# Optimization experiments

Measured on AMD Instinct MI355X. Metric: run time of the kernel, lower is better.

Reference implementation:

```python
import jax, jax.numpy as jnp
import numpy as np

P = 16         # patch size
D = 192        # embed dim (vit_tiny)
NH = 3         # heads
DEPTH = 12
HID = 768      # mlp hidden = 4*D
NCLS = 1000
PCT = 0.25
EPS = 1e-6


def _ln(x, s, b):
    m = x.mean(-1, keepdims=True)
    v = ((x - m) ** 2).mean(-1, keepdims=True)
    return (x - m) * jax.lax.rsqrt(v + EPS) * s + b


def setup_inputs() -> dict:
    key = jax.random.key(0)
    ks = jax.random.split(key, 24)
    B, IMG = 64, 384
    std = 0.02
    d = {
        "magno_image": jax.random.normal(ks[0], (B, 3, IMG, IMG), jnp.float32),
        "line_drawing": jax.random.uniform(ks[1], (B, 1, IMG, IMG), jnp.float32),
        "conv_w": jax.random.normal(ks[2], (D, 3, P, P), jnp.float32) * std,
        "conv_b": jnp.zeros((D,), jnp.float32),
        "pos_embed": jax.random.normal(ks[3], (1, (IMG // P) ** 2 + 1, D), jnp.float32) * std,
        "cls_token": jax.random.normal(ks[4], (1, 1, D), jnp.float32) * std,
        "ln1_s": jnp.ones((DEPTH, D), jnp.float32),
        "ln1_b": jnp.zeros((DEPTH, D), jnp.float32),
        "qkv_w": jax.random.normal(ks[5], (DEPTH, D, 3 * D), jnp.float32) * std,
        "qkv_b": jnp.zeros((DEPTH, 3 * D), jnp.float32),
        "proj_w": jax.random.normal(ks[6], (DEPTH, D, D), jnp.float32) * std,
        "proj_b": jnp.zeros((DEPTH, D), jnp.float32),
        "ln2_s": jnp.ones((DEPTH, D), jnp.float32),
        "ln2_b": jnp.zeros((DEPTH, D), jnp.float32),
        "fc1_w": jax.random.normal(ks[7], (DEPTH, D, HID), jnp.float32) * std,
        "fc1_b": jnp.zeros((DEPTH, HID), jnp.float32),
        "fc2_w": jax.random.normal(ks[8], (DEPTH, HID, D), jnp.float32) * std,
        "fc2_b": jnp.zeros((DEPTH, D), jnp.float32),
        "normf_s": jnp.ones((D,), jnp.float32),
        "normf_b": jnp.zeros((D,), jnp.float32),
        "head_w": jax.random.normal(ks[9], (D, NCLS), jnp.float32) * std,
        "head_b": jnp.zeros((NCLS,), jnp.float32),
    }
    return d


def _forward(magno_image, line_drawing, conv_w, conv_b, pos_embed, cls_token,
             ln1_s, ln1_b, qkv_w, qkv_b, proj_w, proj_b, ln2_s, ln2_b,
             fc1_w, fc1_b, fc2_w, fc2_b, normf_s, normf_b, head_w, head_b):
    B, _, IMG, _ = magno_image.shape
    g = IMG // P
    N = g * g
    k = int(N * PCT)
    hd = D // NH

    # --- PatchImportanceScorer: avg-pool(patch_size) then flatten ---
    scores = line_drawing.reshape(B, g, P, g, P).mean(axis=(2, 4)).reshape(B, N)

    # --- patch embed (conv stride == kernel == reshaped matmul) ---
    x = magno_image.reshape(B, 3, g, P, g, P).transpose(0, 2, 4, 1, 3, 5)
    patches = x.reshape(B, N, 3 * P * P) @ conv_w.reshape(D, 3 * P * P).T + conv_b

    # --- top_k selection + gather of patches and pos-embed ---
    _, idx = jax.lax.top_k(scores, k)                      # (B, k)
    sel = jnp.take_along_axis(patches, idx[:, :, None], axis=1)
    pos = jnp.take_along_axis(
        jnp.broadcast_to(pos_embed[:, 1:, :], (B, N, D)), idx[:, :, None], axis=1)
    sel = sel + pos

    cls = jnp.broadcast_to(cls_token + pos_embed[:, :1, :], (B, 1, D))
    seq = jnp.concatenate([cls, sel], axis=1)              # (B, 1+k, D)
    S = 1 + k

    def block(h, p):
        l1s, l1b, qw, qb, pw, pb, l2s, l2b, f1w, f1b, f2w, f2b = p
        y = _ln(h, l1s, l1b)
        qkv = (y @ qw + qb).reshape(B, S, 3, NH, hd)
        q, kk, v = qkv[:, :, 0], qkv[:, :, 1], qkv[:, :, 2]  # (B,S,NH,hd)
        att = jnp.einsum('bqhd,bkhd->bhqk', q, kk) / np.sqrt(hd).astype(np.float32)
        att = jax.nn.softmax(att, axis=-1)
        o = jnp.einsum('bhqk,bkhd->bqhd', att, v).reshape(B, S, D)
        h = h + o @ pw + pb
        y = _ln(h, l2s, l2b)
        h = h + jax.nn.gelu(y @ f1w + f1b, approximate=False) @ f2w + f2b
        return h, None

    seq, _ = jax.lax.scan(block, seq, (ln1_s, ln1_b, qkv_w, qkv_b, proj_w, proj_b,
                                       ln2_s, ln2_b, fc1_w, fc1_b, fc2_w, fc2_b))
    seq = _ln(seq, normf_s, normf_b)
    return seq[:, 0] @ head_w + head_b


def reference(magno_image, line_drawing, conv_w, conv_b, pos_embed, cls_token,
              ln1_s, ln1_b, qkv_w, qkv_b, proj_w, proj_b, ln2_s, ln2_b,
              fc1_w, fc1_b, fc2_w, fc2_b, normf_s, normf_b, head_w, head_b):
    return _forward(magno_image, line_drawing, conv_w, conv_b, pos_embed, cls_token,
                    ln1_s, ln1_b, qkv_w, qkv_b, proj_w, proj_b, ln2_s, ln2_b,
                    fc1_w, fc1_b, fc2_w, fc2_b, normf_s, normf_b, head_w, head_b)
```

## Files before the change

### kernel.cpp

```cpp
#include <hip/hip_runtime.h>
#include <hip/hip_bf16.h>
#include <cmath>


#define Bsz   64
#define NPATCH 576
#define KSEL  144
#define SEQ   145
#define DIM   192
#define HIDN  768

typedef __bf16 bf16x8 __attribute__((ext_vector_type(8)));
typedef float  f32x4  __attribute__((ext_vector_type(4)));

__global__ __launch_bounds__(256) void scores_kernel(const float* __restrict__ line,
                                                     float* __restrict__ scores)
{
    int gp = blockIdx.x;
    int b = gp / NPATCH, p = gp % NPATCH;
    int gy = p / 24, gx = p % 24;
    int t = threadIdx.x, py = t >> 4, px = t & 15;
    float v = line[((size_t)b * 384 + gy * 16 + py) * 384 + gx * 16 + px];
    for (int off = 32; off; off >>= 1) v += __shfl_xor(v, off);
    __shared__ float red[4];
    if ((t & 63) == 0) red[t >> 6] = v;
    __syncthreads();
    if (t == 0) scores[gp] = (red[0] + red[1] + red[2] + red[3]) * (1.f / 256.f);
}

__global__ __launch_bounds__(256) void topk_kernel(const float* __restrict__ scores,
                                                   int* __restrict__ idx)
{
    int b = blockIdx.x;
    __shared__ float s[NPATCH];
    for (int i = threadIdx.x; i < NPATCH; i += 256) s[i] = scores[b * NPATCH + i];
    __syncthreads();
    for (int i = threadIdx.x; i < NPATCH; i += 256) {
        float si = s[i];
        int cnt = 0;
        for (int j = 0; j < NPATCH; ++j) {
            float sj = s[j];
            cnt += (sj > si) || (sj == si && j < i);
        }
        if (cnt < KSEL) idx[b * KSEL + cnt] = i;
    }
}

__global__ __launch_bounds__(256) void gather_kernel(const float* __restrict__ magno,
                                                     const int* __restrict__ idx,
                                                     __hip_bfloat16* __restrict__ selp)
{
    int bs = blockIdx.x;
    int b = bs / KSEL;
    int pi = idx[bs];
    int gy = pi / 24, gx = pi % 24;
    int t = threadIdx.x, py = t >> 4, px = t & 15;
    size_t src = ((size_t)b * 3 * 384 + gy * 16 + py) * 384 + gx * 16 + px;
    __hip_bfloat16* dst = &selp[(size_t)bs * 768];
#pragma unroll
    for (int c = 0; c < 3; ++c)
        dst[c * 256 + t] = __float2bfloat16(magno[src + (size_t)c * 384 * 384]);
}

__global__ __launch_bounds__(256) void convert_bf16_kernel(const float* __restrict__ src,
                                                           __hip_bfloat16* __restrict__ dst,
                                                           int n)
{
    int i = blockIdx.x * 256 + threadIdx.x;
    if (i < n) dst[i] = __float2bfloat16(src[i]);
}

__global__ __launch_bounds__(256) void transpose_w_kernel(const float* __restrict__ src,
                                                          __hip_bfloat16* __restrict__ dst,
                                                          int R, int C)
{
    __shared__ float t[32][33];
    size_t lo = (size_t)blockIdx.z * R * C;
    int r0 = blockIdx.y * 32, c0 = blockIdx.x * 32;
    int tx = threadIdx.x & 31, ty = threadIdx.x >> 5;
#pragma unroll
    for (int i = 0; i < 32; i += 8)
        t[ty + i][tx] = src[lo + (size_t)(r0 + ty + i) * C + c0 + tx];
    __syncthreads();
#pragma unroll
    for (int i = 0; i < 32; i += 8)
        dst[lo + (size_t)(c0 + ty + i) * R + r0 + tx] = __float2bfloat16(t[tx][ty + i]);
}

__global__ void cls_kernel(const float* __restrict__ cls, const float* __restrict__ pos,
                           float* __restrict__ h)
{
    int b = blockIdx.x, t = threadIdx.x;
    h[(size_t)b * SEQ * DIM + t] = cls[t] + pos[t];
}

__global__ __launch_bounds__(256) void ln_kernel(const float* __restrict__ x,
                                                 const float* __restrict__ s,
                                                 const float* __restrict__ bia,
                                                 __hip_bfloat16* __restrict__ y, int ntok)
{
    int w = threadIdx.x >> 6, lane = threadIdx.x & 63;
    int tok = blockIdx.x * 4 + w;
    if (tok >= ntok) return;
    const float* xp = &x[(size_t)tok * DIM];
    float x0 = xp[lane], x1 = xp[lane + 64], x2 = xp[lane + 128];
    float sum = x0 + x1 + x2;
    for (int off = 32; off; off >>= 1) sum += __shfl_xor(sum, off);
    float mean = sum * (1.f / 192.f);
    float d0 = x0 - mean, d1 = x1 - mean, d2 = x2 - mean;
    float vs = d0 * d0 + d1 * d1 + d2 * d2;
    for (int off = 32; off; off >>= 1) vs += __shfl_xor(vs, off);
    float rs = rsqrtf(vs * (1.f / 192.f) + 1e-6f);
    __hip_bfloat16* yp = &y[(size_t)tok * DIM];
    yp[lane]       = __float2bfloat16(d0 * rs * s[lane]       + bia[lane]);
    yp[lane + 64]  = __float2bfloat16(d1 * rs * s[lane + 64]  + bia[lane + 64]);
    yp[lane + 128] = __float2bfloat16(d2 * rs * s[lane + 128] + bia[lane + 128]);
}

__global__ __launch_bounds__(256) void gemm_embed(const __hip_bfloat16* __restrict__ A,
                                                  const __hip_bfloat16* __restrict__ Wt,
                                                  const float* __restrict__ bias,
                                                  float* __restrict__ h,
                                                  int K,
                                                  const int* __restrict__ selidx,
                                                  const float* __restrict__ pos)
{
    __shared__ __align__(16) char As[8192];
    __shared__ __align__(16) char Bs[8192];
    const int tid = threadIdx.x;
    const int lane = tid & 63, wid = tid >> 6;
    const int wr = wid >> 1, wc = wid & 1;
    const int lr = lane & 15, lk = lane >> 4;
    const int m0 = blockIdx.y * 64, n0 = blockIdx.x * 64;
    f32x4 acc[2][2] = {};

    for (int k0 = 0; k0 < K; k0 += 64) {
#pragma unroll
        for (int it = 0; it < 2; ++it) {
            int chunk = it * 256 + tid;
            int r = chunk >> 3, g = chunk & 7;
            int loff = r * 128 + ((g ^ (r & 7)) * 16);
            *reinterpret_cast<uint4*>(As + loff) =
                *reinterpret_cast<const uint4*>(&A[(size_t)(m0 + r) * K + k0 + g * 8]);
            *reinterpret_cast<uint4*>(Bs + loff) =
                *reinterpret_cast<const uint4*>(&Wt[(size_t)(n0 + r) * K + k0 + g * 8]);
        }
        __syncthreads();
#pragma unroll
        for (int kc = 0; kc < 2; ++kc) {
            int g = kc * 4 + lk;
            bf16x8 af[2], bfr[2];
#pragma unroll
            for (int mi = 0; mi < 2; ++mi) {
                int r = wr * 32 + mi * 16 + lr;
                af[mi] = *reinterpret_cast<const bf16x8*>(As + r * 128 + ((g ^ (r & 7)) * 16));
            }
#pragma unroll
            for (int ni = 0; ni < 2; ++ni) {
                int r = wc * 32 + ni * 16 + lr;
                bfr[ni] = *reinterpret_cast<const bf16x8*>(Bs + r * 128 + ((g ^ (r & 7)) * 16));
            }
#pragma unroll
            for (int mi = 0; mi < 2; ++mi)
#pragma unroll
                for (int ni = 0; ni < 2; ++ni)
                    acc[mi][ni] = __builtin_amdgcn_mfma_f32_16x16x32_bf16(
                        af[mi], bfr[ni], acc[mi][ni], 0, 0, 0);
        }
        __syncthreads();
    }

#pragma unroll
    for (int mi = 0; mi < 2; ++mi)
#pragma unroll
    for (int ni = 0; ni < 2; ++ni)
#pragma unroll
    for (int j = 0; j < 4; ++j) {
        int row = m0 + wr * 32 + mi * 16 + (lane >> 4) * 4 + j;
        int col = n0 + wc * 32 + ni * 16 + (lane & 15);
        float v = acc[mi][ni][j] + bias[col];
        int bb2 = row / KSEL, ss = row % KSEL;
        int pi = selidx[row];
        v += pos[(size_t)(1 + pi) * DIM + col];
        h[((size_t)bb2 * SEQ + 1 + ss) * DIM + col] = v;
    }
}

__global__ __launch_bounds__(256) void gemm_qkv(const __hip_bfloat16* __restrict__ A,
                                                const __hip_bfloat16* __restrict__ Wt,
                                                const float* __restrict__ bias,
                                                __hip_bfloat16* __restrict__ qk,
                                                __hip_bfloat16* __restrict__ Vt)
{
    __shared__ __align__(16) char As[8192];
    __shared__ __align__(16) char Bs[8192];
    const int tid = threadIdx.x;
    const int lane = tid & 63, wid = tid >> 6;
    const int wr = wid >> 1, wc = wid & 1;
    const int lr = lane & 15, lk = lane >> 4;
    const int m0 = blockIdx.y * 64, n0 = blockIdx.x * 64;
    const int K = DIM;
    f32x4 acc[2][2] = {};

    for (int k0 = 0; k0 < K; k0 += 64) {
#pragma unroll
        for (int it = 0; it < 2; ++it) {
            int chunk = it * 256 + tid;
            int r = chunk >> 3, g = chunk & 7;
            int loff = r * 128 + ((g ^ (r & 7)) * 16);
            *reinterpret_cast<uint4*>(As + loff) =
                *reinterpret_cast<const uint4*>(&A[(size_t)(m0 + r) * K + k0 + g * 8]);
            *reinterpret_cast<uint4*>(Bs + loff) =
                *reinterpret_cast<const uint4*>(&Wt[(size_t)(n0 + r) * K + k0 + g * 8]);
        }
        __syncthreads();
#pragma unroll
        for (int kc = 0; kc < 2; ++kc) {
            int g = kc * 4 + lk;
            bf16x8 af[2], bfr[2];
#pragma unroll
            for (int mi = 0; mi < 2; ++mi) {
                int r = wr * 32 + mi * 16 + lr;
                af[mi] = *reinterpret_cast<const bf16x8*>(As + r * 128 + ((g ^ (r & 7)) * 16));
            }
#pragma unroll
            for (int ni = 0; ni < 2; ++ni) {
                int r = wc * 32 + ni * 16 + lr;
                bfr[ni] = *reinterpret_cast<const bf16x8*>(Bs + r * 128 + ((g ^ (r & 7)) * 16));
            }
#pragma unroll
            for (int mi = 0; mi < 2; ++mi)
#pragma unroll
                for (int ni = 0; ni < 2; ++ni)
                    acc[mi][ni] = __builtin_amdgcn_mfma_f32_16x16x32_bf16(
                        af[mi], bfr[ni], acc[mi][ni], 0, 0, 0);
        }
        __syncthreads();
    }

#pragma unroll
    for (int mi = 0; mi < 2; ++mi)
#pragma unroll
    for (int ni = 0; ni < 2; ++ni)
#pragma unroll
    for (int j = 0; j < 4; ++j) {
        int row = m0 + wr * 32 + mi * 16 + (lane >> 4) * 4 + j;
        int col = n0 + wc * 32 + ni * 16 + (lane & 15);
        float v = acc[mi][ni][j] + bias[col];
        if (col < 384) {
            qk[(size_t)row * 384 + col] = __float2bfloat16(v);
        } else {
            int c = col - 384;
            int b = row / SEQ, s = row - b * SEQ;
            Vt[((size_t)(b * 3 + (c >> 6)) * 64 + (c & 63)) * 160 + s] = __float2bfloat16(v);
        }
    }
}

__global__ __launch_bounds__(512) void attnproj_fc1_kernel(
    const __hip_bfloat16* __restrict__ qk,
    const __hip_bfloat16* __restrict__ Vt,
    const __hip_bfloat16* __restrict__ Wp,
    const float* __restrict__ pbias,
    float* __restrict__ h,
    const float* __restrict__ ls,
    const float* __restrict__ lb,
    const __hip_bfloat16* __restrict__ W1t,
    const float* __restrict__ b1,
    __hip_bfloat16* __restrict__ tbuf)
{
    const int b = blockIdx.y, qt = blockIdx.x;
    const int tid = threadIdx.x;
    const int w = tid >> 6, lane = tid & 63;
    const int lr = lane & 15, lg = lane >> 4;
    __shared__ __hip_bfloat16 Ps[3][32][168];
    __shared__ __hip_bfloat16 Ot[32][200];
    __shared__ float redsum[4][32];
    __shared__ float redsq[4][32];
    __hip_bfloat16* Yt = &Ps[0][0][0];

    const size_t qbase = (size_t)b * SEQ * 384;
    const int q0 = qt * 32;

    if (w < 6) {
        const int hh = w >> 1, half = w & 1;
        const int qrow = q0 + half * 16;
        bf16x8 aq[2];
#pragma unroll
        for (int ks = 0; ks < 2; ++ks)
            aq[ks] = *reinterpret_cast<const bf16x8*>(
                &qk[qbase + (size_t)(qrow + lr) * 384 + hh * 64 + ks * 32 + lg * 8]);
        f32x4 sc[10] = {};
#pragma unroll
        for (int nf = 0; nf < 10; ++nf) {
            int key = nf * 16 + lr;
#pragma unroll
            for (int ks = 0; ks < 2; ++ks) {
                bf16x8 bk = *reinterpret_cast<const bf16x8*>(
                    &qk[qbase + (size_t)key * 384 + 192 + hh * 64 + ks * 32 + lg * 8]);
                sc[nf] = __builtin_amdgcn_mfma_f32_16x16x32_bf16(aq[ks], bk, sc[nf], 0, 0, 0);
            }
        }
        float mx[4] = {-1e30f, -1e30f, -1e30f, -1e30f};
#pragma unroll
        for (int nf = 0; nf < 10; ++nf) {
            bool valid = nf * 16 + lr < SEQ;
#pragma unroll
            for (int j = 0; j < 4; ++j) {
                float v = valid ? sc[nf][j] * 0.125f : -1e30f;
                sc[nf][j] = v;
                mx[j] = fmaxf(mx[j], v);
            }
        }
#pragma unroll
        for (int j = 0; j < 4; ++j)
            for (int off = 1; off < 16; off <<= 1)
                mx[j] = fmaxf(mx[j], __shfl_xor(mx[j], off));
        float sm[4] = {0.f, 0.f, 0.f, 0.f};
#pragma unroll
        for (int nf = 0; nf < 10; ++nf)
#pragma unroll
            for (int j = 0; j < 4; ++j) {
                float p = __expf(sc[nf][j] - mx[j]);
                sc[nf][j] = p;
                sm[j] += p;
            }
#pragma unroll
        for (int j = 0; j < 4; ++j) {
            for (int off = 1; off < 16; off <<= 1) sm[j] += __shfl_xor(sm[j], off);
            sm[j] = 1.f / sm[j];
        }
#pragma unroll
        for (int nf = 0; nf < 10; ++nf) {
            int key = nf * 16 + lr;
#pragma unroll
            for (int j = 0; j < 4; ++j)
                Ps[hh][half * 16 + lg * 4 + j][key] = __float2bfloat16(sc[nf][j] * sm[j]);
        }
        const __hip_bfloat16* vtb = &Vt[(size_t)(b * 3 + hh) * 64 * 160];
        f32x4 oacc[4] = {};
#pragma unroll
        for (int ks = 0; ks < 5; ++ks) {
            bf16x8 ap = *reinterpret_cast<const bf16x8*>(&Ps[hh][half * 16 + lr][ks * 32 + lg * 8]);
#pragma unroll
            for (int nf = 0; nf < 4; ++nf) {
                bf16x8 bv = *reinterpret_cast<const bf16x8*>(
                    &vtb[(size_t)(nf * 16 + lr) * 160 + ks * 32 + lg * 8]);
                oacc[nf] = __builtin_amdgcn_mfma_f32_16x16x32_bf16(ap, bv, oacc[nf], 0, 0, 0);
            }
        }
#pragma unroll
        for (int nf = 0; nf < 4; ++nf)
#pragma unroll
            for (int j = 0; j < 4; ++j)
                Ot[half * 16 + lg * 4 + j][hh * 64 + nf * 16 + lr] =
                    __float2bfloat16(oacc[nf][j]);
    }
    __syncthreads();

    const int wm = w & 1, wn = w >> 1;
    f32x4 pacc[3] = {};
#pragma unroll
    for (int kk = 0; kk < 6; ++kk) {
        bf16x8 af = *reinterpret_cast<const bf16x8*>(&Ot[wm * 16 + lr][kk * 32 + lg * 8]);
#pragma unroll
        for (int nf = 0; nf < 3; ++nf) {
            int ncol = wn * 48 + nf * 16 + lr;
            bf16x8 bw = *reinterpret_cast<const bf16x8*>(&Wp[(size_t)ncol * 192 + kk * 32 + lg * 8]);
            pacc[nf] = __builtin_amdgcn_mfma_f32_16x16x32_bf16(af, bw, pacc[nf], 0, 0, 0);
        }
    }
    float v[3][4];
    float psum[4] = {}, psq[4] = {};
#pragma unroll
    for (int nf = 0; nf < 3; ++nf) {
        int col = wn * 48 + nf * 16 + lr;
        float bcol = pbias[col];
#pragma unroll
        for (int j = 0; j < 4; ++j) {
            int q = q0 + wm * 16 + lg * 4 + j;
            float res = (q < SEQ) ? h[((size_t)b * SEQ + q) * DIM + col] : 0.f;
            float t = pacc[nf][j] + bcol + res;
            v[nf][j] = t;
            psum[j] += t;
            psq[j] += t * t;
        }
    }
#pragma unroll
    for (int j = 0; j < 4; ++j) {
        for (int off = 1; off < 16; off <<= 1) {
            psum[j] += __shfl_xor(psum[j], off);
            psq[j]  += __shfl_xor(psq[j], off);
        }
        if (lr == 0) {
            redsum[wn][wm * 16 + lg * 4 + j] = psum[j];
            redsq[wn][wm * 16 + lg * 4 + j]  = psq[j];
        }
    }
    __syncthreads();
#pragma unroll
    for (int j = 0; j < 4; ++j) {
        int r = wm * 16 + lg * 4 + j;
        int q = q0 + r;
        float tsum = redsum[0][r] + redsum[1][r] + redsum[2][r] + redsum[3][r];
        float tsq  = redsq[0][r]  + redsq[1][r]  + redsq[2][r]  + redsq[3][r];
        float mean = tsum * (1.f / 192.f);
        float var  = tsq * (1.f / 192.f) - mean * mean;
        float rs = rsqrtf(var + 1e-6f);
#pragma unroll
        for (int nf = 0; nf < 3; ++nf) {
            int col = wn * 48 + nf * 16 + lr;
            float t = v[nf][j];
            float yv = (t - mean) * rs * ls[col] + lb[col];
            Yt[r * 200 + col] = __float2bfloat16(yv);
            if (q < SEQ) h[((size_t)b * SEQ + q) * DIM + col] = t;
        }
    }
    __syncthreads();

    f32x4 facc[2][6] = {};
#pragma unroll
    for (int ks = 0; ks < 6; ++ks) {
        bf16x8 af[2];
#pragma unroll
        for (int mi = 0; mi < 2; ++mi)
            af[mi] = *reinterpret_cast<const bf16x8*>(&Yt[(mi * 16 + lr) * 200 + ks * 32 + lg * 8]);
#pragma unroll
        for (int nf = 0; nf < 6; ++nf) {
            int col = w * 96 + nf * 16 + lr;
            bf16x8 bw = *reinterpret_cast<const bf16x8*>(&W1t[(size_t)col * DIM + ks * 32 + lg * 8]);
#pragma unroll
            for (int mi = 0; mi < 2; ++mi)
                facc[mi][nf] = __builtin_amdgcn_mfma_f32_16x16x32_bf16(
                    af[mi], bw, facc[mi][nf], 0, 0, 0);
        }
    }
#pragma unroll
    for (int mi = 0; mi < 2; ++mi)
#pragma unroll
    for (int nf = 0; nf < 6; ++nf) {
        int col = w * 96 + nf * 16 + lr;
        float bcol = b1[col];
#pragma unroll
        for (int j = 0; j < 4; ++j) {
            int q = q0 + mi * 16 + lg * 4 + j;
            if (q < SEQ) {
                float vv = facc[mi][nf][j] + bcol;
                float ge = 0.5f * vv * (1.f + erff(vv * 0.70710678118654752f));
                tbuf[((size_t)b * SEQ + q) * HIDN + col] = __float2bfloat16(ge);
            }
        }
    }
}

template <bool DO_LN>
__global__ __launch_bounds__(256) void gemm_res_ln(const __hip_bfloat16* __restrict__ A,
                                                   const __hip_bfloat16* __restrict__ Wt,
                                                   const float* __restrict__ bias,
                                                   float* __restrict__ h,
                                                   const float* __restrict__ ls,
                                                   const float* __restrict__ lb,
                                                   __hip_bfloat16* __restrict__ y,
                                                   int K)
{
    __shared__ __align__(16) char As[8192];
    __shared__ __align__(16) char Bs[24576];
    const int tid = threadIdx.x;
    const int lane = tid & 63, w = tid >> 6;
    const int lr = lane & 15, lg = lane >> 4;
    const int m0 = blockIdx.x * 64;
    f32x4 acc[12] = {};

    for (int k0 = 0; k0 < K; k0 += 64) {
        {
            int chunk = tid;
#pragma unroll
            for (int it = 0; it < 2; ++it, chunk += 256) {
                int r = chunk >> 3, g = chunk & 7;
                *reinterpret_cast<uint4*>(As + r * 128 + ((g ^ (r & 7)) * 16)) =
                    *reinterpret_cast<const uint4*>(&A[(size_t)(m0 + r) * K + k0 + g * 8]);
            }
        }
        {
            int chunk = tid;
#pragma unroll
            for (int it = 0; it < 6; ++it, chunk += 256) {
                int r = chunk >> 3, g = chunk & 7;
                *reinterpret_cast<uint4*>(Bs + r * 128 + ((g ^ (r & 7)) * 16)) =
                    *reinterpret_cast<const uint4*>(&Wt[(size_t)r * K + k0 + g * 8]);
            }
        }
        __syncthreads();
#pragma unroll
        for (int kc = 0; kc < 2; ++kc) {
            int g = kc * 4 + lg;
            int ar = w * 16 + lr;
            bf16x8 af = *reinterpret_cast<const bf16x8*>(As + ar * 128 + ((g ^ (ar & 7)) * 16));
#pragma unroll
            for (int nf = 0; nf < 12; ++nf) {
                int br = nf * 16 + lr;
                bf16x8 bfv = *reinterpret_cast<const bf16x8*>(Bs + br * 128 + ((g ^ (br & 7)) * 16));
                acc[nf] = __builtin_amdgcn_mfma_f32_16x16x32_bf16(af, bfv, acc[nf], 0, 0, 0);
            }
        }
        __syncthreads();
    }

    float v[12][4];
    float sum[4] = {0.f, 0.f, 0.f, 0.f};
#pragma unroll
    for (int nf = 0; nf < 12; ++nf) {
        int col = nf * 16 + lr;
#pragma unroll
        for (int j = 0; j < 4; ++j) {
            int row = m0 + w * 16 + lg * 4 + j;
            float t = acc[nf][j] + bias[col] + h[(size_t)row * DIM + col];
            v[nf][j] = t;
            h[(size_t)row * DIM + col] = t;
            sum[j] += t;
        }
    }
    if (DO_LN) {
#pragma unroll
        for (int j = 0; j < 4; ++j)
            for (int off = 1; off < 16; off <<= 1) sum[j] += __shfl_xor(sum[j], off);
        float mean[4], sq[4] = {0.f, 0.f, 0.f, 0.f};
#pragma unroll
        for (int j = 0; j < 4; ++j) mean[j] = sum[j] * (1.f / 192.f);
#pragma unroll
        for (int nf = 0; nf < 12; ++nf)
#pragma unroll
            for (int j = 0; j < 4; ++j) {
                float d = v[nf][j] - mean[j];
                sq[j] += d * d;
            }
#pragma unroll
        for (int j = 0; j < 4; ++j) {
            for (int off = 1; off < 16; off <<= 1) sq[j] += __shfl_xor(sq[j], off);
            sq[j] = rsqrtf(sq[j] * (1.f / 192.f) + 1e-6f);
        }
#pragma unroll
        for (int nf = 0; nf < 12; ++nf) {
            int col = nf * 16 + lr;
            float sc = ls[col], bc = lb[col];
#pragma unroll
            for (int j = 0; j < 4; ++j) {
                int row = m0 + w * 16 + lg * 4 + j;
                y[(size_t)row * DIM + col] =
                    __float2bfloat16((v[nf][j] - mean[j]) * sq[j] * sc + bc);
            }
        }
    }
}

__global__ __launch_bounds__(256) void head_kernel(const float* __restrict__ h,
                                                   const float* __restrict__ nfs,
                                                   const float* __restrict__ nfb,
                                                   const float* __restrict__ hw,
                                                   const float* __restrict__ hb,
                                                   float* __restrict__ out)
{
    int b = blockIdx.x, t = threadIdx.x;
    __shared__ float y[DIM];
    __shared__ float red[4];
    float x = (t < DIM) ? h[(size_t)b * SEQ * DIM + t] : 0.f;
    float sum = x;
    for (int off = 32; off; off >>= 1) sum += __shfl_xor(sum, off);
    if ((t & 63) == 0) red[t >> 6] = sum;
    __syncthreads();
    float mean = (red[0] + red[1] + red[2] + red[3]) * (1.f / 192.f);
    __syncthreads();
    float d = (t < DIM) ? (x - mean) : 0.f;
    float v = d * d;
    for (int off = 32; off; off >>= 1) v += __shfl_xor(v, off);
    if ((t & 63) == 0) red[t >> 6] = v;
    __syncthreads();
    float var = (red[0] + red[1] + red[2] + red[3]) * (1.f / 192.f);
    float rs = rsqrtf(var + 1e-6f);
    if (t < DIM) y[t] = d * rs * nfs[t] + nfb[t];
    __syncthreads();
    for (int n = t; n < 1000; n += 256) {
        float acc = hb[n];
#pragma unroll 8
        for (int k = 0; k < DIM; ++k)
            acc = fmaf(y[k], hw[(size_t)k * 1000 + n], acc);
        out[(size_t)b * 1000 + n] = acc;
    }
}

extern "C" void kernel_launch(void* const* d_in, const int* in_sizes, int n_in,
                              void* d_out, int out_size, void* d_ws, size_t ws_size,
                              hipStream_t stream)
{
    const float* magno  = (const float*)d_in[0];
    const float* line   = (const float*)d_in[1];
    const float* conv_w = (const float*)d_in[2];
    const float* conv_b = (const float*)d_in[3];
    const float* pos    = (const float*)d_in[4];
    const float* cls    = (const float*)d_in[5];
    const float* ln1_s  = (const float*)d_in[6];
    const float* ln1_b  = (const float*)d_in[7];
    const float* qkv_w  = (const float*)d_in[8];
    const float* qkv_b  = (const float*)d_in[9];
    const float* proj_w = (const float*)d_in[10];
    const float* proj_b = (const float*)d_in[11];
    const float* ln2_s  = (const float*)d_in[12];
    const float* ln2_b  = (const float*)d_in[13];
    const float* fc1_w  = (const float*)d_in[14];
    const float* fc1_b  = (const float*)d_in[15];
    const float* fc2_w  = (const float*)d_in[16];
    const float* fc2_b  = (const float*)d_in[17];
    const float* normf_s = (const float*)d_in[18];
    const float* normf_b = (const float*)d_in[19];
    const float* head_w = (const float*)d_in[20];
    const float* head_b = (const float*)d_in[21];
    float* out = (float*)d_out;
    (void)in_sizes; (void)n_in; (void)out_size; (void)ws_size;

    char* ws = (char*)d_ws;
    int*            idx     = (int*)            (ws + 0);
    float*          h       = (float*)          (ws + 147456);
    __hip_bfloat16* y       = (__hip_bfloat16*) (ws + 7274496);
    __hip_bfloat16* qk      = (__hip_bfloat16*) (ws + 10838016);
    __hip_bfloat16* Vt      = (__hip_bfloat16*) (ws + 17965056);
    __hip_bfloat16* tbuf    = (__hip_bfloat16*) (ws + 21897216);
    __hip_bfloat16* wt_qkv  = (__hip_bfloat16*) (ws + 36151296);
    __hip_bfloat16* wt_proj = (__hip_bfloat16*) (ws + 38805504);
    __hip_bfloat16* wt_fc1  = (__hip_bfloat16*) (ws + 39690240);
    __hip_bfloat16* wt_fc2  = (__hip_bfloat16*) (ws + 43229184);
    float*          scoresbuf = (float*)qk;
    __hip_bfloat16* convT     = y;
    __hip_bfloat16* selp      = tbuf;

    hipMemsetAsync(Vt, 0, 3932160, stream);
    transpose_w_kernel<<<dim3(18, 6, 12), 256, 0, stream>>>(qkv_w, wt_qkv, DIM, 576);
    transpose_w_kernel<<<dim3(6, 6, 12),  256, 0, stream>>>(proj_w, wt_proj, DIM, DIM);
    transpose_w_kernel<<<dim3(24, 6, 12), 256, 0, stream>>>(fc1_w, wt_fc1, DIM, HIDN);
    transpose_w_kernel<<<dim3(6, 24, 12), 256, 0, stream>>>(fc2_w, wt_fc2, HIDN, DIM);
    convert_bf16_kernel<<<576, 256, 0, stream>>>(conv_w, convT, DIM * 768);

    scores_kernel<<<Bsz * NPATCH, 256, 0, stream>>>(line, scoresbuf);
    topk_kernel<<<Bsz, 256, 0, stream>>>(scoresbuf, idx);
    gather_kernel<<<Bsz * KSEL, 256, 0, stream>>>(magno, idx, selp);
    cls_kernel<<<Bsz, DIM, 0, stream>>>(cls, pos, h);
    gemm_embed<<<dim3(3, 144), 256, 0, stream>>>(selp, convT, conv_b, h,
                                                 768, idx, pos);

    const int ntok = Bsz * SEQ;
    ln_kernel<<<ntok / 4, 256, 0, stream>>>(h, ln1_s, ln1_b, y, ntok);
    for (int l = 0; l < 12; ++l) {
        gemm_qkv<<<dim3(9, 145), 256, 0, stream>>>(y, wt_qkv + (size_t)l * 576 * DIM,
                                                   qkv_b + l * 576, qk, Vt);
        attnproj_fc1_kernel<<<dim3(5, Bsz), 512, 0, stream>>>(
            qk, Vt, wt_proj + (size_t)l * DIM * DIM, proj_b + l * DIM, h,
            ln2_s + l * DIM, ln2_b + l * DIM,
            wt_fc1 + (size_t)l * HIDN * DIM, fc1_b + l * HIDN, tbuf);
        if (l < 11)
            gemm_res_ln<true><<<145, 256, 0, stream>>>(
                tbuf, wt_fc2 + (size_t)l * DIM * HIDN, fc2_b + l * DIM, h,
                ln1_s + (l + 1) * DIM, ln1_b + (l + 1) * DIM, y, HIDN);
        else
            gemm_res_ln<false><<<145, 256, 0, stream>>>(
                tbuf, wt_fc2 + (size_t)l * DIM * HIDN, fc2_b + l * DIM, h,
                nullptr, nullptr, y, HIDN);
    }
    head_kernel<<<Bsz, 256, 0, stream>>>(h, normf_s, normf_b, head_w, head_b, out);
}
```

Before: 1.140 ms.

## Split fused attention+fc1 kernel into attention-proj kernel and tiled fc1 GEMM

The kernel that fused attention, projection, LN2 and fc1+GELU is split in two. Attention and projection now run in a smaller 256-thread block over 16 query rows, so the grid grows from 5x64 to 10x64 blocks. That block writes the LN2 output to global memory, and a generic templated bf16 GEMM with a GELU epilogue computes fc1 over 12x145 tiles. The aim is more parallelism and better weight reuse for fc1, since each fused block previously reread all fc1 weights from global memory. The cost is an extra kernel launch per layer and a global round trip of the LN2 activations.

```diff
diff --git a/kernel.cpp b/kernel.cpp
--- a/kernel.cpp
+++ b/kernel.cpp
@@ -117,13 +117,14 @@
     yp[lane + 128] = __float2bfloat16(d2 * rs * s[lane + 128] + bia[lane + 128]);
 }
 
-__global__ __launch_bounds__(256) void gemm_embed(const __hip_bfloat16* __restrict__ A,
-                                                  const __hip_bfloat16* __restrict__ Wt,
-                                                  const float* __restrict__ bias,
-                                                  float* __restrict__ h,
-                                                  int K,
-                                                  const int* __restrict__ selidx,
-                                                  const float* __restrict__ pos)
+template <int MODE>
+__global__ __launch_bounds__(256) void gemm_bf16(const __hip_bfloat16* __restrict__ A,
+                                                 const __hip_bfloat16* __restrict__ Wt,
+                                                 const float* __restrict__ bias,
+                                                 void* __restrict__ Cout,
+                                                 int M, int N, int K,
+                                                 const int* __restrict__ selidx,
+                                                 const float* __restrict__ pos)
 {
     __shared__ __align__(16) char As[8192];
     __shared__ __align__(16) char Bs[8192];
@@ -179,10 +180,15 @@
         int row = m0 + wr * 32 + mi * 16 + (lane >> 4) * 4 + j;
         int col = n0 + wc * 32 + ni * 16 + (lane & 15);
         float v = acc[mi][ni][j] + bias[col];
-        int bb2 = row / KSEL, ss = row % KSEL;
-        int pi = selidx[row];
-        v += pos[(size_t)(1 + pi) * DIM + col];
-        h[((size_t)bb2 * SEQ + 1 + ss) * DIM + col] = v;
+        if (MODE == 2) {
+            ((__hip_bfloat16*)Cout)[(size_t)row * N + col] =
+                __float2bfloat16(0.5f * v * (1.f + erff(v * 0.70710678118654752f)));
+        } else {
+            int bb2 = row / KSEL, ss = row % KSEL;
+            int pi = selidx[row];
+            v += pos[(size_t)(1 + pi) * DIM + col];
+            ((float*)Cout)[((size_t)bb2 * SEQ + 1 + ss) * DIM + col] = v;
+        }
     }
 }
 
@@ -257,39 +263,34 @@
     }
 }
 
-__global__ __launch_bounds__(512) void attnproj_fc1_kernel(
-    const __hip_bfloat16* __restrict__ qk,
-    const __hip_bfloat16* __restrict__ Vt,
-    const __hip_bfloat16* __restrict__ Wp,
-    const float* __restrict__ pbias,
-    float* __restrict__ h,
-    const float* __restrict__ ls,
-    const float* __restrict__ lb,
-    const __hip_bfloat16* __restrict__ W1t,
-    const float* __restrict__ b1,
-    __hip_bfloat16* __restrict__ tbuf)
+__global__ __launch_bounds__(256) void attnproj_kernel(const __hip_bfloat16* __restrict__ qk,
+                                                       const __hip_bfloat16* __restrict__ Vt,
+                                                       const __hip_bfloat16* __restrict__ Wp,
+                                                       const float* __restrict__ pbias,
+                                                       float* __restrict__ h,
+                                                       const float* __restrict__ ls,
+                                                       const float* __restrict__ lb,
+                                                       __hip_bfloat16* __restrict__ y)
 {
     const int b = blockIdx.y, qt = blockIdx.x;
     const int tid = threadIdx.x;
     const int w = tid >> 6, lane = tid & 63;
     const int lr = lane & 15, lg = lane >> 4;
-    __shared__ __hip_bfloat16 Ps[3][32][168];
-    __shared__ __hip_bfloat16 Ot[32][200];
-    __shared__ float redsum[4][32];
-    __shared__ float redsq[4][32];
-    __hip_bfloat16* Yt = &Ps[0][0][0];
+    __shared__ __hip_bfloat16 Ps[3][16][168];
+    __shared__ __hip_bfloat16 Ot[16][200];
+    __shared__ float redsum[4][16];
+    __shared__ float redsq[4][16];
 
     const size_t qbase = (size_t)b * SEQ * 384;
-    const int q0 = qt * 32;
-
-    if (w < 6) {
-        const int hh = w >> 1, half = w & 1;
-        const int qrow = q0 + half * 16;
+    const int q0 = qt * 16;
+
+    if (w < 3) {
+        const int hh = w;
         bf16x8 aq[2];
 #pragma unroll
         for (int ks = 0; ks < 2; ++ks)
             aq[ks] = *reinterpret_cast<const bf16x8*>(
-                &qk[qbase + (size_t)(qrow + lr) * 384 + hh * 64 + ks * 32 + lg * 8]);
+                &qk[qbase + (size_t)(q0 + lr) * 384 + hh * 64 + ks * 32 + lg * 8]);
         f32x4 sc[10] = {};
 #pragma unroll
         for (int nf = 0; nf < 10; ++nf) {
@@ -335,13 +336,13 @@
             int key = nf * 16 + lr;
 #pragma unroll
             for (int j = 0; j < 4; ++j)
-                Ps[hh][half * 16 + lg * 4 + j][key] = __float2bfloat16(sc[nf][j] * sm[j]);
+                Ps[hh][lg * 4 + j][key] = __float2bfloat16(sc[nf][j] * sm[j]);
         }
         const __hip_bfloat16* vtb = &Vt[(size_t)(b * 3 + hh) * 64 * 160];
         f32x4 oacc[4] = {};
 #pragma unroll
         for (int ks = 0; ks < 5; ++ks) {
-            bf16x8 ap = *reinterpret_cast<const bf16x8*>(&Ps[hh][half * 16 + lr][ks * 32 + lg * 8]);
+            bf16x8 ap = *reinterpret_cast<const bf16x8*>(&Ps[hh][lr][ks * 32 + lg * 8]);
 #pragma unroll
             for (int nf = 0; nf < 4; ++nf) {
                 bf16x8 bv = *reinterpret_cast<const bf16x8*>(
@@ -353,16 +354,15 @@
         for (int nf = 0; nf < 4; ++nf)
 #pragma unroll
             for (int j = 0; j < 4; ++j)
-                Ot[half * 16 + lg * 4 + j][hh * 64 + nf * 16 + lr] =
-                    __float2bfloat16(oacc[nf][j]);
-    }
-    __syncthreads();
-
-    const int wm = w & 1, wn = w >> 1;
+                Ot[lg * 4 + j][hh * 64 + nf * 16 + lr] = __float2bfloat16(oacc[nf][j]);
+    }
+    __syncthreads();
+
+    const int wn = w;
     f32x4 pacc[3] = {};
 #pragma unroll
     for (int kk = 0; kk < 6; ++kk) {
-        bf16x8 af = *reinterpret_cast<const bf16x8*>(&Ot[wm * 16 + lr][kk * 32 + lg * 8]);
+        bf16x8 af = *reinterpret_cast<const bf16x8*>(&Ot[lr][kk * 32 + lg * 8]);
 #pragma unroll
         for (int nf = 0; nf < 3; ++nf) {
             int ncol = wn * 48 + nf * 16 + lr;
@@ -378,7 +378,7 @@
         float bcol = pbias[col];
 #pragma unroll
         for (int j = 0; j < 4; ++j) {
-            int q = q0 + wm * 16 + lg * 4 + j;
+            int q = q0 + lg * 4 + j;
             float res = (q < SEQ) ? h[((size_t)b * SEQ + q) * DIM + col] : 0.f;
             float t = pacc[nf][j] + bcol + res;
             v[nf][j] = t;
@@ -393,15 +393,16 @@
             psq[j]  += __shfl_xor(psq[j], off);
         }
         if (lr == 0) {
-            redsum[wn][wm * 16 + lg * 4 + j] = psum[j];
-            redsq[wn][wm * 16 + lg * 4 + j]  = psq[j];
+            redsum[wn][lg * 4 + j] = psum[j];
+            redsq[wn][lg * 4 + j]  = psq[j];
         }
     }
     __syncthreads();
 #pragma unroll
     for (int j = 0; j < 4; ++j) {
-        int r = wm * 16 + lg * 4 + j;
+        int r = lg * 4 + j;
         int q = q0 + r;
+        if (q >= SEQ) continue;
         float tsum = redsum[0][r] + redsum[1][r] + redsum[2][r] + redsum[3][r];
         float tsq  = redsq[0][r]  + redsq[1][r]  + redsq[2][r]  + redsq[3][r];
         float mean = tsum * (1.f / 192.f);
@@ -411,44 +412,9 @@
         for (int nf = 0; nf < 3; ++nf) {
             int col = wn * 48 + nf * 16 + lr;
             float t = v[nf][j];
-            float yv = (t - mean) * rs * ls[col] + lb[col];
-            Yt[r * 200 + col] = __float2bfloat16(yv);
-            if (q < SEQ) h[((size_t)b * SEQ + q) * DIM + col] = t;
-        }
-    }
-    __syncthreads();
-
-    f32x4 facc[2][6] = {};
-#pragma unroll
-    for (int ks = 0; ks < 6; ++ks) {
-        bf16x8 af[2];
-#pragma unroll
-        for (int mi = 0; mi < 2; ++mi)
-            af[mi] = *reinterpret_cast<const bf16x8*>(&Yt[(mi * 16 + lr) * 200 + ks * 32 + lg * 8]);
-#pragma unroll
-        for (int nf = 0; nf < 6; ++nf) {
-            int col = w * 96 + nf * 16 + lr;
-            bf16x8 bw = *reinterpret_cast<const bf16x8*>(&W1t[(size_t)col * DIM + ks * 32 + lg * 8]);
-#pragma unroll
-            for (int mi = 0; mi < 2; ++mi)
-                facc[mi][nf] = __builtin_amdgcn_mfma_f32_16x16x32_bf16(
-                    af[mi], bw, facc[mi][nf], 0, 0, 0);
-        }
-    }
-#pragma unroll
-    for (int mi = 0; mi < 2; ++mi)
-#pragma unroll
-    for (int nf = 0; nf < 6; ++nf) {
-        int col = w * 96 + nf * 16 + lr;
-        float bcol = b1[col];
-#pragma unroll
-        for (int j = 0; j < 4; ++j) {
-            int q = q0 + mi * 16 + lg * 4 + j;
-            if (q < SEQ) {
-                float vv = facc[mi][nf][j] + bcol;
-                float ge = 0.5f * vv * (1.f + erff(vv * 0.70710678118654752f));
-                tbuf[((size_t)b * SEQ + q) * HIDN + col] = __float2bfloat16(ge);
-            }
+            h[((size_t)b * SEQ + q) * DIM + col] = t;
+            y[((size_t)b * SEQ + q) * DIM + col] =
+                __float2bfloat16((t - mean) * rs * ls[col] + lb[col]);
         }
     }
 }
@@ -643,18 +609,21 @@
     topk_kernel<<<Bsz, 256, 0, stream>>>(scoresbuf, idx);
     gather_kernel<<<Bsz * KSEL, 256, 0, stream>>>(magno, idx, selp);
     cls_kernel<<<Bsz, DIM, 0, stream>>>(cls, pos, h);
-    gemm_embed<<<dim3(3, 144), 256, 0, stream>>>(selp, convT, conv_b, h,
-                                                 768, idx, pos);
+    gemm_bf16<3><<<dim3(3, 144), 256, 0, stream>>>(selp, convT, conv_b, h,
+                                                   9216, DIM, 768, idx, pos);
 
     const int ntok = Bsz * SEQ;
     ln_kernel<<<ntok / 4, 256, 0, stream>>>(h, ln1_s, ln1_b, y, ntok);
     for (int l = 0; l < 12; ++l) {
         gemm_qkv<<<dim3(9, 145), 256, 0, stream>>>(y, wt_qkv + (size_t)l * 576 * DIM,
                                                    qkv_b + l * 576, qk, Vt);
-        attnproj_fc1_kernel<<<dim3(5, Bsz), 512, 0, stream>>>(
-            qk, Vt, wt_proj + (size_t)l * DIM * DIM, proj_b + l * DIM, h,
-            ln2_s + l * DIM, ln2_b + l * DIM,
-            wt_fc1 + (size_t)l * HIDN * DIM, fc1_b + l * HIDN, tbuf);
+        attnproj_kernel<<<dim3(10, Bsz), 256, 0, stream>>>(qk, Vt,
+                                                           wt_proj + (size_t)l * DIM * DIM,
+                                                           proj_b + l * DIM, h,
+                                                           ln2_s + l * DIM, ln2_b + l * DIM, y);
+        gemm_bf16<2><<<dim3(12, 145), 256, 0, stream>>>(y, wt_fc1 + (size_t)l * HIDN * DIM,
+                                                        fc1_b + l * HIDN, tbuf,
+                                                        ntok, HIDN, DIM, nullptr, nullptr);
         if (l < 11)
             gemm_res_ln<true><<<145, 256, 0, stream>>>(
                 tbuf, wt_fc2 + (size_t)l * DIM * HIDN, fc2_b + l * DIM, h,
```

Measured after the change: 955.3 us. 16.2% less time.
